# Optimization experiments

Hardware: AMD Instinct MI355X
Metric: run time of the kernel (lower is better)

Reference implementation:

```python
import jax, jax.numpy as jnp
import numpy as np

B, CIN, X, Y = 4, 3, 128, 128
D, L, DEPTH, OUT = 64, 8, 4, 1
GRID_RANGE = 1.0
LN_EPS = 1e-5
YR = Y // 2 + 1


def _build_phi_f():
    # 1D Hilbert-matrix eigenbases along each axis, outer product, then rfft2.
    def top_eigvecs(n):
        i = np.arange(n)
        Z = 1.0 / (i[:, None] + i[None, :] + 1.0)  # Hilbert matrix, float64
        w, V = np.linalg.eigh(Z)
        idx = np.argsort(-w)[:L]
        return V.T[idx]  # (L, n)

    Vx = top_eigvecs(X)
    Vy = top_eigvecs(Y)
    phi = Vx[:, :, None] * Vy[:, None, :]  # (L, X, Y) separable eigenfunctions
    Phi_f = np.fft.rfft2(phi, s=(X, Y))  # (L, X, YR)
    return jnp.asarray(Phi_f, dtype=jnp.complex64)


def setup_inputs() -> dict:
    key = jax.random.key(0)
    ks = jax.random.split(key, 16)
    u = lambda k, shape, bound: jax.random.uniform(k, shape, jnp.float32, -bound, bound)
    inv = 1.0 / np.sqrt(D)
    inp = {
        "x": jax.random.normal(ks[0], (B, CIN, X, Y), jnp.float32),
        "Phi_f": _build_phi_f(),  # constant buffer
        "lift_w": u(ks[1], (D, CIN + 2), 1.0 / np.sqrt(CIN + 2)),
        "lift_b": u(ks[2], (D,), 1.0 / np.sqrt(CIN + 2)),
        "Theta": u(ks[3], (DEPTH, L, D, D), 1.0 / D),  # kaiming_uniform(a=sqrt(5)) ~ U(-1/d, 1/d)
        "glu_val_w": u(ks[4], (DEPTH, D, D), inv),
        "glu_val_b": u(ks[5], (DEPTH, D), inv),
        "glu_gate_w": u(ks[6], (DEPTH, D, D), inv),
        "glu_gate_b": u(ks[7], (DEPTH, D), inv),
        "ln_g": jnp.ones((DEPTH, D), jnp.float32),
        "ln_b": jnp.zeros((DEPTH, D), jnp.float32),
        "head_w": u(ks[8], (OUT, D), inv),
        "head_b": u(ks[9], (OUT,), inv),
    }
    return inp


def _stu_layer(h, Phi_f, Theta, vw, vb, gw, gb, g, b):
    # LayerNorm over channel dim (torch LayerNorm on channels-last view)
    ht = jnp.transpose(h, (0, 2, 3, 1))  # (B, X, Y, D)
    mu = jnp.mean(ht, axis=-1, keepdims=True)
    var = jnp.var(ht, axis=-1, keepdims=True)
    zt = (ht - mu) * jax.lax.rsqrt(var + LN_EPS) * g + b
    z = jnp.transpose(zt, (0, 3, 1, 2))  # (B, D, X, Y)

    Xf = jnp.fft.rfftn(z, axes=(-2, -1))  # (B, D, X, YR) complex
    Uf = Xf[:, :, None, :, :] * jnp.conj(Phi_f)[None, None]  # (B, D, L, X, YR)
    U = jnp.fft.irfftn(Uf, s=(X, Y), axes=(-2, -1))  # (B, D, L, X, Y)
    # einsum('bdlxy,lhd->bhlxy') followed by sum over l, fused:
    S = jnp.einsum("bdlxy,lhd->bhxy", U, Theta)

    V = jnp.einsum("bhxy,oh->boxy", S, vw) + vb[None, :, None, None]
    G = jax.nn.sigmoid(jnp.einsum("bhxy,oh->boxy", S, gw) + gb[None, :, None, None])
    return h + V * G


def reference(x, Phi_f, lift_w, lift_b, Theta, glu_val_w, glu_val_b,
              glu_gate_w, glu_gate_b, ln_g, ln_b, head_w, head_b):
    bsz = x.shape[0]
    # add_2d_grid: append yy, xx coordinate channels
    ys = jnp.linspace(0.0, GRID_RANGE, X, dtype=x.dtype)
    xs = jnp.linspace(0.0, GRID_RANGE, Y, dtype=x.dtype)
    yy, xx = jnp.meshgrid(ys, xs, indexing="ij")
    yy = jnp.broadcast_to(yy[None, None], (bsz, 1, X, Y))
    xx = jnp.broadcast_to(xx[None, None], (bsz, 1, X, Y))
    h = jnp.concatenate([x, yy, xx], axis=1)  # (B, CIN+2, X, Y)

    # LocalLift2D with kernel_size=1 -> pointwise conv
    h = jnp.einsum("bcxy,dc->bdxy", h, lift_w) + lift_b[None, :, None, None]

    for i in range(DEPTH):
        h = _stu_layer(h, Phi_f, Theta[i], glu_val_w[i], glu_val_b[i],
                       glu_gate_w[i], glu_gate_b[i], ln_g[i], ln_b[i])

    y = jnp.einsum("bdxy,od->boxy", h, head_w) + head_b[None, :, None, None]
    return y
```

## Files before the change

kernel.cpp:

```cpp
#include <hip/hip_runtime.h>
#include <math.h>
#include <string.h>


#define NXY 16384

#define OFF_V       16
#define OFF_MC      1040
#define OFF_THETAA  132112
#define OFF_AG      263184
#define OFF_Z       295952
#define OFF_H       4490256
#define OFF_P       8684560
#define WS_NEED_F   25461776ULL

typedef short short8 __attribute__((ext_vector_type(8)));
typedef float float4m __attribute__((ext_vector_type(4)));

__device__ __forceinline__ unsigned short bf_rn(float f) {
    unsigned u = __float_as_uint(f);
    u += 0x7fffu + ((u >> 16) & 1u);
    return (unsigned short)(u >> 16);
}
__device__ __forceinline__ float bf_tof(unsigned short s) {
    return __uint_as_float(((unsigned)s) << 16);
}

__global__ void poison_out(float* out) { out[0] = 1e9f; }


static float vhost[1024];

static void host_hilbert_topk(float* outv) {
    static double Vs[8][128];
    static double W[8][128];
    double recip[256];
    for (int i = 0; i < 256; i++) recip[i] = 1.0 / (double)(i + 1);
    for (int j = 0; j < 8; j++)
        for (int i = 0; i < 128; i++) Vs[j][i] = recip[i + j];
    for (int outer = 0; outer < 25; outer++) {
        for (int half = 0; half < 2; half++) {
            for (int j = 0; j < 8; j++)
                for (int i = 0; i < 128; i++) {
                    double s = 0.0;
                    for (int k = 0; k < 128; k++) s += Vs[j][k] * recip[i + k];
                    W[j][i] = s;
                }
            memcpy(Vs, W, sizeof(Vs));
        }
        for (int j = 0; j < 8; j++) {
            for (int p = 0; p < j; p++) {
                double d = 0.0;
                for (int i = 0; i < 128; i++) d += Vs[j][i] * Vs[p][i];
                for (int i = 0; i < 128; i++) Vs[j][i] -= d * Vs[p][i];
            }
            double nn = 0.0;
            for (int i = 0; i < 128; i++) nn += Vs[j][i] * Vs[j][i];
            double inv = 1.0 / sqrt(nn);
            for (int i = 0; i < 128; i++) Vs[j][i] *= inv;
        }
    }
    for (int j = 0; j < 8; j++)
        for (int i = 0; i < 128; i++) outv[j * 128 + i] = (float)Vs[j][i];
}

namespace {
struct VInit {
    VInit() { host_hilbert_topk(vhost); }
};
VInit vinit_once;
}

__global__ void build_mct(const float* __restrict__ v, unsigned short* __restrict__ McT) {
    int l = blockIdx.y;
    int idx = blockIdx.x * 256 + threadIdx.x;
    int r = idx >> 7, k = idx & 127;
    McT[l * 16384 + idx] = bf_rn(v[l * 128 + ((k - r) & 127)]);
}


__global__ void build_thetaAHL(const float* __restrict__ Theta, unsigned short* __restrict__ ThA) {
    int i = blockIdx.x * 256 + threadIdx.x;
    int k = i & 127; int r = i >> 7;
    int m = r & 127; r >>= 7;
    int tile = r & 3; int dep = r >> 2;
    int l2 = m >> 6, hch = m & 63, d = k & 63;
    float f = Theta[(((dep * 8 + tile * 2 + l2) * 64) + hch) * 64 + d];
    unsigned short hb = bf_rn(f);
    ThA[i] = (k < 64) ? hb : bf_rn(f - bf_tof(hb));
}

__global__ void build_AG(const float* __restrict__ vw, const float* __restrict__ gw,
                         float* __restrict__ AG) {
    int i = blockIdx.x * 256 + threadIdx.x;
    int m = i & 127; int r = i >> 7; int h = r & 63; int dep = r >> 6;
    int o = m >> 1;
    const float* W = (m & 1) ? gw : vw;
    AG[i] = W[(dep * 64 + o) * 64 + h];
}


__global__ void lift_ln(const float* __restrict__ x, const float* __restrict__ lw,
                        const float* __restrict__ lb, const float* __restrict__ g0,
                        const float* __restrict__ b0, float* __restrict__ h,
                        unsigned short* __restrict__ zT) {
    __shared__ float w[320];
    __shared__ float bsm[64];
    __shared__ float gs[64], bs[64];
    int tid = threadIdx.x;
    for (int i = tid; i < 320; i += 256) w[i] = lw[i];
    if (tid < 64) { bsm[tid] = lb[tid]; gs[tid] = g0[tid]; bs[tid] = b0[tid]; }
    __syncthreads();
    int b = blockIdx.y;
    int xy = blockIdx.x * 256 + tid;
    int xi = xy >> 7, yi = xy & 127;
    float c0 = x[(size_t)(b * 3 + 0) * NXY + xy];
    float c1 = x[(size_t)(b * 3 + 1) * NXY + xy];
    float c2 = x[(size_t)(b * 3 + 2) * NXY + xy];
    float yyv = xi * (1.0f / 127.0f), xxv = yi * (1.0f / 127.0f);
    float vv[64];
    float sum = 0.f;
#pragma unroll
    for (int d = 0; d < 64; d++) {
        float acc = bsm[d] + w[d * 5] * c0 + w[d * 5 + 1] * c1 + w[d * 5 + 2] * c2
                  + w[d * 5 + 3] * yyv + w[d * 5 + 4] * xxv;
        vv[d] = acc;
        sum += acc;
        h[(size_t)(b * 64 + d) * NXY + xy] = acc;
    }
    float mu = sum * (1.0f / 64.0f);
    float vs = 0.f;
#pragma unroll
    for (int d = 0; d < 64; d++) { float t = vv[d] - mu; vs += t * t; }
    float inv = rsqrtf(vs * (1.0f / 64.0f) + 1e-5f);
    unsigned short t16[64];
#pragma unroll
    for (int d = 0; d < 64; d++) t16[d] = bf_rn((vv[d] - mu) * inv * gs[d] + bs[d]);
    unsigned short* zp = zT + ((size_t)b * NXY + xy) * 64;
#pragma unroll
    for (int i = 0; i < 8; i++) {
        uint4 pk;
        pk.x = (unsigned)t16[8 * i + 0] | ((unsigned)t16[8 * i + 1] << 16);
        pk.y = (unsigned)t16[8 * i + 2] | ((unsigned)t16[8 * i + 3] << 16);
        pk.z = (unsigned)t16[8 * i + 4] | ((unsigned)t16[8 * i + 5] << 16);
        pk.w = (unsigned)t16[8 * i + 6] | ((unsigned)t16[8 * i + 7] << 16);
        *(uint4*)(zp + 8 * i) = pk;
    }
}

__device__ __forceinline__ int sw_idx(int row, int k) {
    return row * 128 + ((((k >> 3) ^ (row & 7)) << 3) | (k & 7));
}


__launch_bounds__(256)
__global__ void k1_mfma(const unsigned short* __restrict__ zT,
                        const unsigned short* __restrict__ ThA,
                        unsigned short* __restrict__ P) {
    __shared__ unsigned short st[16384];
    const int lhtile = blockIdx.x, x = blockIdx.y, b = blockIdx.z;
    const int tid = threadIdx.x;
    const int wid = tid >> 6, lane = tid & 63;
    const int ln15 = lane & 15, q = lane >> 4;
    const int ko = q * 8;
    const unsigned short* Ab = ThA + lhtile * 16384;
    const unsigned short* Bb = zT + ((size_t)b * NXY + x * 128) * 64;

    float4m acc[2][8];
#pragma unroll
    for (int mt = 0; mt < 2; mt++)
#pragma unroll
        for (int nt = 0; nt < 8; nt++) acc[mt][nt] = (float4m){0.f, 0.f, 0.f, 0.f};

#pragma unroll
    for (int k0 = 0; k0 < 128; k0 += 32) {
        short8 a[2];
#pragma unroll
        for (int mt = 0; mt < 2; mt++)
            a[mt] = *(const short8*)(Ab + (wid * 32 + mt * 16 + ln15) * 128 + k0 + ko);
        int d0 = (k0 & 63) + ko;
#pragma unroll
        for (int nt = 0; nt < 8; nt++) {
            int n = nt * 16 + ln15;
            short8 bf = *(const short8*)(Bb + n * 64 + d0);
#pragma unroll
            for (int mt = 0; mt < 2; mt++)
                acc[mt][nt] = __builtin_amdgcn_mfma_f32_16x16x32_bf16(a[mt], bf, acc[mt][nt], 0, 0, 0);
        }
    }
#pragma unroll
    for (int mt = 0; mt < 2; mt++)
#pragma unroll
        for (int nt = 0; nt < 8; nt++) {
            int y = nt * 16 + ln15;
            int r0 = wid * 32 + mt * 16 + q * 4;
            float av[4] = {acc[mt][nt].x, acc[mt][nt].y, acc[mt][nt].z, acc[mt][nt].w};
#pragma unroll
            for (int r = 0; r < 4; r++) st[sw_idx(r0 + r, y)] = bf_rn(av[r]);
        }
    __syncthreads();
    unsigned short* Pb = P + (size_t)(b * 512 + lhtile * 128) * NXY + x * 128;
#pragma unroll
    for (int i = 0; i < 8; i++) {
        int idx = i * 256 + tid;
        int m = idx >> 4, c = idx & 15;
        *(uint4*)(Pb + (size_t)m * NXY + c * 8) = *(const uint4*)&st[sw_idx(m, c * 8)];
    }
}


__launch_bounds__(256)
__global__ void corr2q(unsigned short* __restrict__ P,
                       const unsigned short* __restrict__ McT) {
    __shared__ unsigned short Tt[16384];
    const int hh = blockIdx.x, l = blockIdx.y, b = blockIdx.z;
    unsigned short* plane = P + ((size_t)(b * 8 + l) * 64 + hh) * NXY;
    const unsigned short* Mc = McT + l * 16384;
    const int tid = threadIdx.x;
    const int wid = tid >> 6, lane = tid & 63;
    const int ln15 = lane & 15, q = lane >> 4;
    const int ko = q * 8;

    float4m acc[2][8];
#pragma unroll
    for (int mt = 0; mt < 2; mt++)
#pragma unroll
        for (int nt = 0; nt < 8; nt++) acc[mt][nt] = (float4m){0.f, 0.f, 0.f, 0.f};

#pragma unroll
    for (int k0 = 0; k0 < 128; k0 += 32) {
        short8 a[2];
#pragma unroll
        for (int mt = 0; mt < 2; mt++)
            a[mt] = *(const short8*)(plane + (wid * 32 + mt * 16 + ln15) * 128 + k0 + ko);
#pragma unroll
        for (int nt = 0; nt < 8; nt++) {
            int n = nt * 16 + ln15;
            short8 bf = *(const short8*)(Mc + n * 128 + k0 + ko);
#pragma unroll
            for (int mt = 0; mt < 2; mt++)
                acc[mt][nt] = __builtin_amdgcn_mfma_f32_16x16x32_bf16(a[mt], bf, acc[mt][nt], 0, 0, 0);
        }
    }
#pragma unroll
    for (int mt = 0; mt < 2; mt++)
#pragma unroll
        for (int nt = 0; nt < 8; nt++) {
            int yo = nt * 16 + ln15;
            int x0 = wid * 32 + mt * 16 + q * 4;
            float av[4] = {acc[mt][nt].x, acc[mt][nt].y, acc[mt][nt].z, acc[mt][nt].w};
            unsigned short hs[4];
#pragma unroll
            for (int r = 0; r < 4; r++) hs[r] = bf_rn(av[r]);
            uint2 pk;
            pk.x = (unsigned)hs[0] | ((unsigned)hs[1] << 16);
            pk.y = (unsigned)hs[2] | ((unsigned)hs[3] << 16);
            *(uint2*)&Tt[sw_idx(yo, x0)] = pk;
        }
    __syncthreads();

#pragma unroll
    for (int mt = 0; mt < 2; mt++)
#pragma unroll
        for (int nt = 0; nt < 8; nt++) acc[mt][nt] = (float4m){0.f, 0.f, 0.f, 0.f};
#pragma unroll
    for (int k0 = 0; k0 < 128; k0 += 32) {
        short8 a[2];
#pragma unroll
        for (int mt = 0; mt < 2; mt++)
            a[mt] = *(const short8*)(Mc + (wid * 32 + mt * 16 + ln15) * 128 + k0 + ko);
#pragma unroll
        for (int nt = 0; nt < 8; nt++) {
            int n = nt * 16 + ln15;
            short8 bf = *(const short8*)&Tt[sw_idx(n, k0 + ko)];
#pragma unroll
            for (int mt = 0; mt < 2; mt++)
                acc[mt][nt] = __builtin_amdgcn_mfma_f32_16x16x32_bf16(a[mt], bf, acc[mt][nt], 0, 0, 0);
        }
    }
    __syncthreads();
#pragma unroll
    for (int mt = 0; mt < 2; mt++)
#pragma unroll
        for (int nt = 0; nt < 8; nt++) {
            int y = nt * 16 + ln15;
            int x0 = wid * 32 + mt * 16 + q * 4;
            float av[4] = {acc[mt][nt].x, acc[mt][nt].y, acc[mt][nt].z, acc[mt][nt].w};
#pragma unroll
            for (int r = 0; r < 4; r++) Tt[sw_idx(x0 + r, y)] = bf_rn(av[r]);
        }
    __syncthreads();
#pragma unroll
    for (int i = 0; i < 8; i++) {
        int idx = i * 256 + tid;
        int xr = idx >> 4, c = idx & 15;
        *(uint4*)(plane + xr * 128 + c * 8) = *(const uint4*)&Tt[sw_idx(xr, c * 8)];
    }
}


template <int KTOT, long long BS1, long long PSTR, int NPART>
__launch_bounds__(256)
__global__ void glu_ln(const float* __restrict__ A0,
                       const unsigned short* __restrict__ B0, long long bsx, long long bsz,
                       float* __restrict__ C0, long long csx, long long csz, long long csm,
                       const float* __restrict__ e_vb, const float* __restrict__ e_gb,
                       const float* __restrict__ lngn, const float* __restrict__ lnbn,
                       unsigned short* __restrict__ zT,
                       const float* __restrict__ hw, const float* __restrict__ hbp,
                       float* __restrict__ outp) {
    constexpr int KS = 16;
    __shared__ float As[KS][132];
    __shared__ float Bs[KS][132];
    __shared__ float hn[64][129];
    const int tid = threadIdx.x;
    const int tm = tid >> 4, tn = tid & 15;
    const int m0 = tm * 8, n0 = tn * 8;
    const float* Ab = A0;
    const unsigned short* Bb = B0 + (long long)blockIdx.x * bsx + (long long)blockIdx.z * bsz;
    float* Cb = C0 + (long long)blockIdx.x * csx + (long long)blockIdx.z * csz;

    float acc[8][8];
#pragma unroll
    for (int i = 0; i < 8; i++)
#pragma unroll
        for (int j = 0; j < 8; j++) acc[i][j] = 0.f;

    for (int k0 = 0; k0 < KTOT; k0 += KS) {
#pragma unroll
        for (int i = 0; i < 2; i++) {
            int idx = tid + i * 256;
            int k = idx >> 5, f4 = (idx & 31) * 4;
            float4 v = *(const float4*)(Ab + (long long)(k0 + k) * 128 + f4);
            *(float4*)&As[k][f4] = v;
        }
#pragma unroll
        for (int i = 0; i < 2; i++) {
            int idx = tid + i * 256;
            int k = idx >> 5, f4 = (idx & 31) * 4;
            const unsigned short* bp = Bb + (long long)(k0 + k) * BS1 + f4;
            float vx = 0.f, vy = 0.f, vz = 0.f, vw = 0.f;
#pragma unroll
            for (int p = 0; p < NPART; p++) {
                uint2 t = *(const uint2*)(bp + (long long)p * PSTR);
                vx += bf_tof((unsigned short)(t.x & 0xffff));
                vy += bf_tof((unsigned short)(t.x >> 16));
                vz += bf_tof((unsigned short)(t.y & 0xffff));
                vw += bf_tof((unsigned short)(t.y >> 16));
            }
            Bs[k][f4] = vx; Bs[k][f4 + 1] = vy; Bs[k][f4 + 2] = vz; Bs[k][f4 + 3] = vw;
        }
        __syncthreads();
#pragma unroll
        for (int kk = 0; kk < KS; kk++) {
            float4 a0 = *(const float4*)&As[kk][m0];
            float4 a1 = *(const float4*)&As[kk][m0 + 4];
            float4 b0 = *(const float4*)&Bs[kk][n0];
            float4 b1 = *(const float4*)&Bs[kk][n0 + 4];
            float av[8] = {a0.x, a0.y, a0.z, a0.w, a1.x, a1.y, a1.z, a1.w};
            float bv[8] = {b0.x, b0.y, b0.z, b0.w, b1.x, b1.y, b1.z, b1.w};
#pragma unroll
            for (int i = 0; i < 8; i++)
#pragma unroll
                for (int j = 0; j < 8; j++) acc[i][j] += av[i] * bv[j];
        }
        __syncthreads();
    }

#pragma unroll
    for (int i = 0; i < 4; i++) {
        int o = (m0 >> 1) + i;
        float vbv = e_vb[o], gbv = e_gb[o];
        float* hp = Cb + (long long)o * csm + n0;
        float4 h0 = *(float4*)hp;
        float4 h1 = *(float4*)(hp + 4);
        float hv[8] = {h0.x, h0.y, h0.z, h0.w, h1.x, h1.y, h1.z, h1.w};
#pragma unroll
        for (int j = 0; j < 8; j++) {
            float V = acc[2 * i][j] + vbv;
            float G = acc[2 * i + 1][j] + gbv;
            float s = 1.0f / (1.0f + expf(-G));
            hv[j] += V * s;
            hn[o][n0 + j] = hv[j];
        }
        if (outp == nullptr) {
            float4 o0 = {hv[0], hv[1], hv[2], hv[3]};
            float4 o1 = {hv[4], hv[5], hv[6], hv[7]};
            *(float4*)hp = o0;
            *(float4*)(hp + 4) = o1;
        }
    }

    if (lngn != nullptr) {
        __syncthreads();
        if (tid < 128) {
            int xy = tid;
            float sum = 0.f;
#pragma unroll
            for (int d = 0; d < 64; d++) sum += hn[d][xy];
            float mu = sum * (1.0f / 64.0f);
            float vs = 0.f;
#pragma unroll
            for (int d = 0; d < 64; d++) { float t = hn[d][xy] - mu; vs += t * t; }
            float inv = rsqrtf(vs * (1.0f / 64.0f) + 1e-5f);
            unsigned short t16[64];
#pragma unroll
            for (int d = 0; d < 64; d++)
                t16[d] = bf_rn((hn[d][xy] - mu) * inv * lngn[d] + lnbn[d]);
            unsigned short* zp = zT + ((size_t)blockIdx.z * NXY + blockIdx.x * 128 + xy) * 64;
#pragma unroll
            for (int i = 0; i < 8; i++) {
                uint4 pk;
                pk.x = (unsigned)t16[8 * i + 0] | ((unsigned)t16[8 * i + 1] << 16);
                pk.y = (unsigned)t16[8 * i + 2] | ((unsigned)t16[8 * i + 3] << 16);
                pk.z = (unsigned)t16[8 * i + 4] | ((unsigned)t16[8 * i + 5] << 16);
                pk.w = (unsigned)t16[8 * i + 6] | ((unsigned)t16[8 * i + 7] << 16);
                *(uint4*)(zp + 8 * i) = pk;
            }
        }
    } else if (outp != nullptr) {
        __syncthreads();
        if (tid < 128) {
            int xy = tid;
            float acch = hbp[0];
#pragma unroll
            for (int d = 0; d < 64; d++) acch += hn[d][xy] * hw[d];
            outp[(size_t)blockIdx.z * NXY + blockIdx.x * 128 + xy] = acch;
        }
    }
}


extern "C" void kernel_launch(void* const* d_in, const int* in_sizes, int n_in,
                              void* d_out, int out_size, void* d_ws, size_t ws_size,
                              hipStream_t stream) {
    const float* x      = (const float*)d_in[0];
    const float* lift_w = (const float*)d_in[2];
    const float* lift_b = (const float*)d_in[3];
    const float* Theta  = (const float*)d_in[4];
    const float* vw     = (const float*)d_in[5];
    const float* vb     = (const float*)d_in[6];
    const float* gw     = (const float*)d_in[7];
    const float* gb     = (const float*)d_in[8];
    const float* ln_g   = (const float*)d_in[9];
    const float* ln_b   = (const float*)d_in[10];
    const float* head_w = (const float*)d_in[11];
    const float* head_b = (const float*)d_in[12];
    float* out = (float*)d_out;
    float* ws = (float*)d_ws;
    (void)in_sizes; (void)n_in; (void)out_size;

    float* v      = ws + OFF_V;
    unsigned short* McT = (unsigned short*)(ws + OFF_MC);
    unsigned short* ThA = (unsigned short*)(ws + OFF_THETAA);
    float* AG     = ws + OFF_AG;
    unsigned short* zT = (unsigned short*)(ws + OFF_Z);
    float* h      = ws + OFF_H;
    unsigned short* P = (unsigned short*)(ws + OFF_P);

    hipMemcpyAsync(v, vhost, sizeof(vhost), hipMemcpyHostToDevice, stream);

    build_mct<<<dim3(64, 8), 256, 0, stream>>>(v, McT);
    build_thetaAHL<<<1024, 256, 0, stream>>>(Theta, ThA);
    build_AG<<<128, 256, 0, stream>>>(vw, gw, AG);

    lift_ln<<<dim3(64, 4), 256, 0, stream>>>(x, lift_w, lift_b, ln_g, ln_b, h, zT);

    for (int dep = 0; dep < 4; dep++) {
        k1_mfma<<<dim3(4, 128, 4), 256, 0, stream>>>(zT, ThA + dep * 65536, P);

        corr2q<<<dim3(64, 8, 4), 256, 0, stream>>>(P, McT);

        const float* lngn = (dep < 3) ? (ln_g + (dep + 1) * 64) : nullptr;
        const float* lnbn = (dep < 3) ? (ln_b + (dep + 1) * 64) : nullptr;
        float* outp = (dep == 3) ? out : nullptr;
        glu_ln<64, 16384LL, 1048576LL, 8><<<dim3(128, 1, 4), 256, 0, stream>>>(
            AG + dep * 8192,
            P, 128, 8388608,
            h, 128, 1048576, 16384,
            vb + dep * 64, gb + dep * 64,
            lngn, lnbn, zT,
            head_w, head_b, outp);
    }

    if (ws_size < WS_NEED_F * 4ULL) {
        poison_out<<<1, 1, 0, stream>>>(out);
    }
}
```

Before: 589.1 us.

## Fuse the sum over L into the correlation kernel and write one S plane

The correlation kernel now loops over all 8 spectral filters inside one block and accumulates the second GEMM across them in registers. It writes a single summed S plane per (b,h) instead of 8 per-filter planes, and the GLU kernel reads S with one partition instead of summing 8. The next filter's P tile is prefetched into registers while the current one is processed. This cuts global writes and the GLU read traffic by about 8x. The cost is that the grid shrinks from 2048 to 256 blocks, which lowers parallelism on a large GPU, and register pressure rises from the prefetch buffers.

```diff
diff --git a/kernel.cpp b/kernel.cpp
--- a/kernel.cpp
+++ b/kernel.cpp
@@ -10,6 +10,7 @@
 #define OFF_THETAA  132112
 #define OFF_AG      263184
 #define OFF_Z       295952
+#define OFF_S       2393104
 #define OFF_H       4490256
 #define OFF_P       8684560
 #define WS_NEED_F   25461776ULL
@@ -210,91 +211,118 @@
 
 
 __launch_bounds__(256)
-__global__ void corr2q(unsigned short* __restrict__ P,
-                       const unsigned short* __restrict__ McT) {
+__global__ void corrsum(const unsigned short* __restrict__ P,
+                        const unsigned short* __restrict__ McT,
+                        unsigned short* __restrict__ S) {
     __shared__ unsigned short Tt[16384];
-    const int hh = blockIdx.x, l = blockIdx.y, b = blockIdx.z;
-    unsigned short* plane = P + ((size_t)(b * 8 + l) * 64 + hh) * NXY;
-    const unsigned short* Mc = McT + l * 16384;
+    const int hh = blockIdx.x, b = blockIdx.y;
     const int tid = threadIdx.x;
     const int wid = tid >> 6, lane = tid & 63;
     const int ln15 = lane & 15, q = lane >> 4;
     const int ko = q * 8;
-
-    float4m acc[2][8];
+    const int mrow0 = wid * 32 + ln15;
+
+    float4m accS[2][8];
 #pragma unroll
     for (int mt = 0; mt < 2; mt++)
 #pragma unroll
-        for (int nt = 0; nt < 8; nt++) acc[mt][nt] = (float4m){0.f, 0.f, 0.f, 0.f};
-
-#pragma unroll
-    for (int k0 = 0; k0 < 128; k0 += 32) {
-        short8 a[2];
+        for (int nt = 0; nt < 8; nt++) accS[mt][nt] = (float4m){0.f, 0.f, 0.f, 0.f};
+
+    short8 apre[2][4][2];
+
+    {
+        const unsigned short* pl = P + ((size_t)(b * 8 + 0) * 64 + hh) * NXY;
+#pragma unroll
+        for (int k4 = 0; k4 < 4; k4++)
+#pragma unroll
+            for (int mt = 0; mt < 2; mt++)
+                apre[0][k4][mt] = *(const short8*)(pl + (mrow0 + mt * 16) * 128 + k4 * 32 + ko);
+    }
+
+#pragma unroll
+    for (int l = 0; l < 8; l++) {
+        const unsigned short* Mc = McT + l * 16384;
+        const int cb = l & 1, nb = cb ^ 1;
+
+        float4m acc1[2][8];
 #pragma unroll
         for (int mt = 0; mt < 2; mt++)
-            a[mt] = *(const short8*)(plane + (wid * 32 + mt * 16 + ln15) * 128 + k0 + ko);
-#pragma unroll
-        for (int nt = 0; nt < 8; nt++) {
-            int n = nt * 16 + ln15;
-            short8 bf = *(const short8*)(Mc + n * 128 + k0 + ko);
+#pragma unroll
+            for (int nt = 0; nt < 8; nt++) acc1[mt][nt] = (float4m){0.f, 0.f, 0.f, 0.f};
+#pragma unroll
+        for (int k4 = 0; k4 < 4; k4++) {
+            int k0 = k4 * 32;
+#pragma unroll
+            for (int nt = 0; nt < 8; nt++) {
+                int n = nt * 16 + ln15;
+                short8 bf = *(const short8*)(Mc + n * 128 + k0 + ko);
+#pragma unroll
+                for (int mt = 0; mt < 2; mt++)
+                    acc1[mt][nt] = __builtin_amdgcn_mfma_f32_16x16x32_bf16(apre[cb][k4][mt], bf, acc1[mt][nt], 0, 0, 0);
+            }
+        }
+#pragma unroll
+        for (int mt = 0; mt < 2; mt++)
+#pragma unroll
+            for (int nt = 0; nt < 8; nt++) {
+                int yo = nt * 16 + ln15;
+                int x0 = wid * 32 + mt * 16 + q * 4;
+                float av[4] = {acc1[mt][nt].x, acc1[mt][nt].y, acc1[mt][nt].z, acc1[mt][nt].w};
+                unsigned short hs[4];
+#pragma unroll
+                for (int r = 0; r < 4; r++) hs[r] = bf_rn(av[r]);
+                uint2 pk;
+                pk.x = (unsigned)hs[0] | ((unsigned)hs[1] << 16);
+                pk.y = (unsigned)hs[2] | ((unsigned)hs[3] << 16);
+                *(uint2*)&Tt[sw_idx(yo, x0)] = pk;
+            }
+        __syncthreads();
+
+        if (l < 7) {
+            const unsigned short* pln = P + ((size_t)(b * 8 + l + 1) * 64 + hh) * NXY;
+#pragma unroll
+            for (int k4 = 0; k4 < 4; k4++)
+#pragma unroll
+                for (int mt = 0; mt < 2; mt++)
+                    apre[nb][k4][mt] = *(const short8*)(pln + (mrow0 + mt * 16) * 128 + k4 * 32 + ko);
+        }
+
+#pragma unroll
+        for (int k4 = 0; k4 < 4; k4++) {
+            int k0 = k4 * 32;
+            short8 a2[2];
 #pragma unroll
             for (int mt = 0; mt < 2; mt++)
-                acc[mt][nt] = __builtin_amdgcn_mfma_f32_16x16x32_bf16(a[mt], bf, acc[mt][nt], 0, 0, 0);
-        }
-    }
-#pragma unroll
-    for (int mt = 0; mt < 2; mt++)
-#pragma unroll
-        for (int nt = 0; nt < 8; nt++) {
-            int yo = nt * 16 + ln15;
-            int x0 = wid * 32 + mt * 16 + q * 4;
-            float av[4] = {acc[mt][nt].x, acc[mt][nt].y, acc[mt][nt].z, acc[mt][nt].w};
-            unsigned short hs[4];
-#pragma unroll
-            for (int r = 0; r < 4; r++) hs[r] = bf_rn(av[r]);
-            uint2 pk;
-            pk.x = (unsigned)hs[0] | ((unsigned)hs[1] << 16);
-            pk.y = (unsigned)hs[2] | ((unsigned)hs[3] << 16);
-            *(uint2*)&Tt[sw_idx(yo, x0)] = pk;
-        }
-    __syncthreads();
-
-#pragma unroll
-    for (int mt = 0; mt < 2; mt++)
-#pragma unroll
-        for (int nt = 0; nt < 8; nt++) acc[mt][nt] = (float4m){0.f, 0.f, 0.f, 0.f};
-#pragma unroll
-    for (int k0 = 0; k0 < 128; k0 += 32) {
-        short8 a[2];
-#pragma unroll
-        for (int mt = 0; mt < 2; mt++)
-            a[mt] = *(const short8*)(Mc + (wid * 32 + mt * 16 + ln15) * 128 + k0 + ko);
-#pragma unroll
-        for (int nt = 0; nt < 8; nt++) {
-            int n = nt * 16 + ln15;
-            short8 bf = *(const short8*)&Tt[sw_idx(n, k0 + ko)];
-#pragma unroll
-            for (int mt = 0; mt < 2; mt++)
-                acc[mt][nt] = __builtin_amdgcn_mfma_f32_16x16x32_bf16(a[mt], bf, acc[mt][nt], 0, 0, 0);
-        }
-    }
-    __syncthreads();
+                a2[mt] = *(const short8*)(Mc + (mrow0 + mt * 16) * 128 + k0 + ko);
+#pragma unroll
+            for (int nt = 0; nt < 8; nt++) {
+                int n = nt * 16 + ln15;
+                short8 bf = *(const short8*)&Tt[sw_idx(n, k0 + ko)];
+#pragma unroll
+                for (int mt = 0; mt < 2; mt++)
+                    accS[mt][nt] = __builtin_amdgcn_mfma_f32_16x16x32_bf16(a2[mt], bf, accS[mt][nt], 0, 0, 0);
+            }
+        }
+        __syncthreads();
+    }
+
 #pragma unroll
     for (int mt = 0; mt < 2; mt++)
 #pragma unroll
         for (int nt = 0; nt < 8; nt++) {
             int y = nt * 16 + ln15;
             int x0 = wid * 32 + mt * 16 + q * 4;
-            float av[4] = {acc[mt][nt].x, acc[mt][nt].y, acc[mt][nt].z, acc[mt][nt].w};
+            float av[4] = {accS[mt][nt].x, accS[mt][nt].y, accS[mt][nt].z, accS[mt][nt].w};
 #pragma unroll
             for (int r = 0; r < 4; r++) Tt[sw_idx(x0 + r, y)] = bf_rn(av[r]);
         }
     __syncthreads();
+    unsigned short* Sb = S + ((size_t)(b * 64) + hh) * NXY;
 #pragma unroll
     for (int i = 0; i < 8; i++) {
         int idx = i * 256 + tid;
         int xr = idx >> 4, c = idx & 15;
-        *(uint4*)(plane + xr * 128 + c * 8) = *(const uint4*)&Tt[sw_idx(xr, c * 8)];
+        *(uint4*)(Sb + xr * 128 + c * 8) = *(const uint4*)&Tt[sw_idx(xr, c * 8)];
     }
 }
 
@@ -455,6 +483,7 @@
     unsigned short* ThA = (unsigned short*)(ws + OFF_THETAA);
     float* AG     = ws + OFF_AG;
     unsigned short* zT = (unsigned short*)(ws + OFF_Z);
+    unsigned short* S  = (unsigned short*)(ws + OFF_S);
     float* h      = ws + OFF_H;
     unsigned short* P = (unsigned short*)(ws + OFF_P);
 
@@ -469,14 +498,14 @@
     for (int dep = 0; dep < 4; dep++) {
         k1_mfma<<<dim3(4, 128, 4), 256, 0, stream>>>(zT, ThA + dep * 65536, P);
 
-        corr2q<<<dim3(64, 8, 4), 256, 0, stream>>>(P, McT);
+        corrsum<<<dim3(64, 4), 256, 0, stream>>>(P, McT, S);
 
         const float* lngn = (dep < 3) ? (ln_g + (dep + 1) * 64) : nullptr;
         const float* lnbn = (dep < 3) ? (ln_b + (dep + 1) * 64) : nullptr;
         float* outp = (dep == 3) ? out : nullptr;
-        glu_ln<64, 16384LL, 1048576LL, 8><<<dim3(128, 1, 4), 256, 0, stream>>>(
+        glu_ln<64, 16384LL, 0LL, 1><<<dim3(128, 1, 4), 256, 0, stream>>>(
             AG + dep * 8192,
-            P, 128, 8388608,
+            S, 128, 1048576,
             h, 128, 1048576, 16384,
             vb + dep * 64, gb + dep * 64,
             lngn, lnbn, zT,
```

Measured after the change: 637.3 us. 1.08x slower.
